# Performance work log

Hardware: AMD Instinct MI355X
Metric: run time of the kernel (lower is better)

The kernel has to match this reference:

```python
import math
import jax, jax.numpy as jnp
import numpy as np

N = 65536   # total nodes across episodes
H = 512     # hidden size
B = 4096    # number of episodes / decoding items
M = 32      # max neighbors (padded ragged valid_actions)


def setup_inputs() -> dict:
    key = jax.random.key(0)
    ks = jax.random.split(key, 9)
    s = 1.0 / math.sqrt(H)
    return {
        "h_static": jax.random.normal(ks[0], (N, H), jnp.float32),
        "h_dynamic": jax.random.normal(ks[1], (N, H), jnp.float32),
        "Ws_kvl": jax.random.normal(ks[2], (H, 3 * H), jnp.float32) * s,
        "Wd_kvl": jax.random.normal(ks[3], (H, 3 * H), jnp.float32) * s,
        "Wq": jax.random.normal(ks[4], (H, H), jnp.float32) * s,
        "batch": jax.random.randint(ks[5], (N,), 0, B, jnp.int32),
        "current_nodes": jax.random.randint(ks[6], (B,), 0, N),
        "neigh_idx": jax.random.randint(ks[7], (B, M), 0, N),
        "lengths": jax.random.randint(ks[8], (B,), 0, M + 1),
    }


def reference(h_static, h_dynamic, Ws_kvl, Wd_kvl, Wq, batch, current_nodes, neigh_idx, lengths):
    # precompute(): static KVL projection (full 3H GEMM then chunk, as in torch)
    kvl_s = h_static @ Ws_kvl            # [N, 3H]
    K_s = kvl_s[:, :H]
    # forward_batch(): dynamic projection
    kvl_d = h_dynamic @ Wd_kvl           # [N, 3H]
    K_d = kvl_d[:, :H]
    K = K_s + K_d                        # [N, H]  (V is computed but unused for outputs)
    q = (h_static[current_nodes] + h_dynamic[current_nodes]) @ Wq  # [B, H]

    # padded ragged neighbor attention (replaces the Python loop over B)
    Kn = K[neigh_idx]                                        # [B, M, H]
    compat = jnp.einsum('bmh,bh->bm', Kn, q) / math.sqrt(H)  # [B, M]
    mask = jnp.arange(M)[None, :] < lengths[:, None]         # [B, M]
    NEG = jnp.float32(-1e9)
    logits = jnp.where(mask, compat, NEG)

    # categorical sampling via Gumbel-max (Categorical(logits).sample())
    u = jax.random.uniform(jax.random.key(1), (B, M), jnp.float32, 1e-8, 1.0)
    g = -jnp.log(-jnp.log(u))
    idx = jnp.argmax(logits + g, axis=-1)                    # [B]

    logp = jax.nn.log_softmax(logits, axis=-1)               # [B, M]
    lp = jnp.take_along_axis(logp, idx[:, None], axis=1)[:, 0]
    actions = jnp.take_along_axis(neigh_idx, idx[:, None], axis=1)[:, 0]

    # empty neighbor list -> stay at current node, log_prob 0 (matches torch branch)
    nonempty = lengths > 0
    actions = jnp.where(nonempty, actions, current_nodes)
    lp = jnp.where(nonempty, lp, jnp.float32(0.0))
    return actions, lp
```

## Files before the change

kernel.cpp:

```cpp
#include <hip/hip_runtime.h>
#include <cstdint>
#include <cstddef>

#define HDIM 512
#define NM 32
#define NBATCH 4096

__device__ __forceinline__ unsigned rotl32(unsigned x, unsigned d) {
  return (x << d) | (x >> (32u - d));
}

__device__ __forceinline__ void threefry2x32(unsigned& x0, unsigned& x1) {
  const unsigned ks0 = 0u, ks1 = 1u, ks2 = 0x1BD11BDBu;
  x0 += ks0; x1 += ks1;
#define TF_RND(r) { x0 += x1; x1 = rotl32(x1, (r)); x1 ^= x0; }
  TF_RND(13) TF_RND(15) TF_RND(26) TF_RND(6)
  x0 += ks1; x1 += ks2 + 1u;
  TF_RND(17) TF_RND(29) TF_RND(16) TF_RND(24)
  x0 += ks2; x1 += ks0 + 2u;
  TF_RND(13) TF_RND(15) TF_RND(26) TF_RND(6)
  x0 += ks0; x1 += ks1 + 3u;
  TF_RND(17) TF_RND(29) TF_RND(16) TF_RND(24)
  x0 += ks1; x1 += ks2 + 4u;
  TF_RND(13) TF_RND(15) TF_RND(26) TF_RND(6)
  x0 += ks2; x1 += ks0 + 5u;
#undef TF_RND
}

__global__ void gather_hc(const float* __restrict__ hs,
                          const float* __restrict__ hd,
                          const int* __restrict__ cur,
                          float* __restrict__ Hc) {
  const int b = blockIdx.x;
  const int t = threadIdx.x;
  const int n = cur[b];
  const float4 a = ((const float4*)(hs + (size_t)n * HDIM))[t];
  const float4 c = ((const float4*)(hd + (size_t)n * HDIM))[t];
  float4 r;
  r.x = a.x + c.x; r.y = a.y + c.y; r.z = a.z + c.z; r.w = a.w + c.w;
  ((float4*)(Hc + (size_t)b * HDIM))[t] = r;
}

__global__ __launch_bounds__(256) void gemm_b1(const float* __restrict__ Ws,
                                               const float* __restrict__ Wd,
                                               const float* __restrict__ Wq,
                                               float* __restrict__ M2T) {
  constexpr int BK = 16, LDT = 68;
  __shared__ float Ast[BK][LDT];
  __shared__ float Bst[BK][LDT];
  const int tid = threadIdx.x;
  const int row0 = blockIdx.y * 64;
  const int col0 = blockIdx.x * 64;
  const float* Abase = (row0 < 512) ? Ws : Wd;
  const int arow0 = (row0 < 512) ? row0 : row0 - 512;
  const int tx = tid & 15, ty = tid >> 4;
  const int lr = tid >> 2, lc = (tid & 3) * 4;
  float acc[4][4] = {};
  for (int k0 = 0; k0 < 512; k0 += BK) {
    float4 va = *(const float4*)(Abase + (size_t)(arow0 + lr) * 1536 + k0 + lc);
    float4 vb = *(const float4*)(Wq + (size_t)(col0 + lr) * 512 + k0 + lc);
    Ast[lc + 0][lr] = va.x; Ast[lc + 1][lr] = va.y;
    Ast[lc + 2][lr] = va.z; Ast[lc + 3][lr] = va.w;
    Bst[lc + 0][lr] = vb.x; Bst[lc + 1][lr] = vb.y;
    Bst[lc + 2][lr] = vb.z; Bst[lc + 3][lr] = vb.w;
    __syncthreads();
#pragma unroll
    for (int k = 0; k < BK; ++k) {
      float4 a4 = *(const float4*)&Ast[k][ty * 4];
      float4 b4 = *(const float4*)&Bst[k][tx * 4];
      float a[4] = {a4.x, a4.y, a4.z, a4.w};
      float bb[4] = {b4.x, b4.y, b4.z, b4.w};
#pragma unroll
      for (int i = 0; i < 4; ++i)
#pragma unroll
        for (int j = 0; j < 4; ++j) acc[i][j] += a[i] * bb[j];
    }
    __syncthreads();
  }
#pragma unroll
  for (int i = 0; i < 4; ++i) {
    float4 o;
    o.x = acc[i][0]; o.y = acc[i][1]; o.z = acc[i][2]; o.w = acc[i][3];
    *(float4*)(M2T + (size_t)(row0 + ty * 4 + i) * 512 + col0 + tx * 4) = o;
  }
}

__global__ __launch_bounds__(256) void gemm_v(const float* __restrict__ A,
                                              const float* __restrict__ Bm,
                                              float* __restrict__ C) {
  constexpr int BK = 16, LDT = 132;
  __shared__ float Ast[BK][LDT];
  __shared__ float Bst[BK][LDT];
  const int tid = threadIdx.x;
  const int row0 = blockIdx.y * 128;
  const int col0 = blockIdx.x * 128;
  const int tx = tid & 15, ty = tid >> 4;
  const int lr = tid >> 2, lc = (tid & 3) * 4;
  float acc[8][8] = {};
  for (int k0 = 0; k0 < 512; k0 += BK) {
#pragma unroll
    for (int h = 0; h < 2; ++h) {
      const int r = lr + h * 64;
      float4 va = *(const float4*)(A + (size_t)(row0 + r) * 512 + k0 + lc);
      float4 vb = *(const float4*)(Bm + (size_t)(col0 + r) * 512 + k0 + lc);
      Ast[lc + 0][r] = va.x; Ast[lc + 1][r] = va.y;
      Ast[lc + 2][r] = va.z; Ast[lc + 3][r] = va.w;
      Bst[lc + 0][r] = vb.x; Bst[lc + 1][r] = vb.y;
      Bst[lc + 2][r] = vb.z; Bst[lc + 3][r] = vb.w;
    }
    __syncthreads();
#pragma unroll
    for (int k = 0; k < BK; ++k) {
      float4 a0 = *(const float4*)&Ast[k][ty * 8];
      float4 a1 = *(const float4*)&Ast[k][ty * 8 + 4];
      float4 b0 = *(const float4*)&Bst[k][tx * 8];
      float4 b1 = *(const float4*)&Bst[k][tx * 8 + 4];
      float a[8] = {a0.x, a0.y, a0.z, a0.w, a1.x, a1.y, a1.z, a1.w};
      float bb[8] = {b0.x, b0.y, b0.z, b0.w, b1.x, b1.y, b1.z, b1.w};
#pragma unroll
      for (int i = 0; i < 8; ++i)
#pragma unroll
        for (int j = 0; j < 8; ++j) acc[i][j] += a[i] * bb[j];
    }
    __syncthreads();
  }
#pragma unroll
  for (int i = 0; i < 8; ++i) {
    float4 o0, o1;
    o0.x = acc[i][0]; o0.y = acc[i][1]; o0.z = acc[i][2]; o0.w = acc[i][3];
    o1.x = acc[i][4]; o1.y = acc[i][5]; o1.z = acc[i][6]; o1.w = acc[i][7];
    float* cp = C + (size_t)(row0 + ty * 8 + i) * 1024 + col0 + tx * 8;
    *(float4*)cp = o0;
    *(float4*)(cp + 4) = o1;
  }
}

__global__ __launch_bounds__(256) void attend_kernel(
    const float* __restrict__ hs, const float* __restrict__ hd,
    const float* __restrict__ V, const int* __restrict__ neigh,
    const int* __restrict__ lengths, const int* __restrict__ cur,
    float* __restrict__ out) {
  const int b = blockIdx.x;
  const int tid = threadIdx.x;
  const int lane = tid & 63;
  const int wave = tid >> 6;
  __shared__ float compat[NM];

  const float4* vrow = (const float4*)(V + (size_t)b * (2 * HDIM));
  const float4 w0 = vrow[lane * 2], w1 = vrow[lane * 2 + 1];
  const float4 u0 = vrow[128 + lane * 2], u1 = vrow[128 + lane * 2 + 1];

#pragma unroll
  for (int mi = 0; mi < 8; ++mi) {
    const int m = wave * 8 + mi;
    const int n = neigh[b * NM + m];
    const float4* a4 = (const float4*)(hs + (size_t)n * HDIM);
    const float4* c4 = (const float4*)(hd + (size_t)n * HDIM);
    const float4 a0 = a4[lane * 2], a1 = a4[lane * 2 + 1];
    const float4 b0 = c4[lane * 2], b1 = c4[lane * 2 + 1];
    float acc = a0.x * w0.x + a0.y * w0.y + a0.z * w0.z + a0.w * w0.w
              + a1.x * w1.x + a1.y * w1.y + a1.z * w1.z + a1.w * w1.w
              + b0.x * u0.x + b0.y * u0.y + b0.z * u0.z + b0.w * u0.w
              + b1.x * u1.x + b1.y * u1.y + b1.z * u1.z + b1.w * u1.w;
#pragma unroll
    for (int off = 32; off >= 1; off >>= 1) acc += __shfl_xor(acc, off);
    if (lane == 0) compat[m] = acc;
  }
  __syncthreads();

  if (tid < 64) {
    const int len = lengths[b];
    const bool valid = tid < NM;
    const float NEGMAX = -3.402823466e38f;
    float logit = NEGMAX;
    if (valid) {
      const float cm = compat[tid] / 22.62741699796952f;
      logit = (tid < len) ? cm : -1e9f;
    }
    float z = NEGMAX;
    int zi = 1 << 20;
    if (valid) {
      const unsigned i_lo = (unsigned)b * 32u + (unsigned)tid;
      unsigned x0 = 0u;
      unsigned x1 = i_lo;
      threefry2x32(x0, x1);
      const unsigned bits = x0 ^ x1;
      const float fu = __uint_as_float((bits >> 9) | 0x3f800000u) - 1.0f;
      const float uu = fmaxf(1e-8f, fu + 1e-8f);
      const float g = -logf(-logf(uu));
      z = logit + g;
      zi = tid;
    }
#pragma unroll
    for (int off = 32; off >= 1; off >>= 1) {
      const float oz = __shfl_xor(z, off);
      const int oi = __shfl_xor(zi, off);
      if (oz > z || (oz == z && oi < zi)) { z = oz; zi = oi; }
    }
    float ml = logit;
#pragma unroll
    for (int off = 32; off >= 1; off >>= 1) ml = fmaxf(ml, __shfl_xor(ml, off));
    float ex = valid ? expf(logit - ml) : 0.f;
#pragma unroll
    for (int off = 32; off >= 1; off >>= 1) ex += __shfl_xor(ex, off);
    const float lsel = __shfl(logit, zi);
    if (tid == 0) {
      float lp = lsel - ml - logf(ex);
      int act = neigh[b * NM + zi];
      if (len <= 0) { act = cur[b]; lp = 0.f; }
      out[b] = (float)act;
      out[NBATCH + b] = lp;
    }
  }
}

extern "C" void kernel_launch(void* const* d_in, const int* in_sizes, int n_in,
                              void* d_out, int out_size, void* d_ws, size_t ws_size,
                              hipStream_t stream) {
  const float* hs = (const float*)d_in[0];
  const float* hd = (const float*)d_in[1];
  const float* Ws = (const float*)d_in[2];
  const float* Wd = (const float*)d_in[3];
  const float* Wq = (const float*)d_in[4];
  const int* cur = (const int*)d_in[6];
  const int* neigh = (const int*)d_in[7];
  const int* lens = (const int*)d_in[8];
  float* out = (float*)d_out;

  char* ws = (char*)d_ws;
  float* Hc  = (float*)ws;
  float* M2T = (float*)(ws + (size_t)NBATCH * HDIM * 4);
  float* V   = (float*)(ws + (size_t)NBATCH * HDIM * 4 + (size_t)1024 * 512 * 4);

  hipLaunchKernelGGL(gemm_b1, dim3(8, 16), dim3(256), 0, stream, Ws, Wd, Wq, M2T);
  hipLaunchKernelGGL(gather_hc, dim3(NBATCH), dim3(128), 0, stream, hs, hd, cur, Hc);
  hipLaunchKernelGGL(gemm_v, dim3(8, 32), dim3(256), 0, stream, Hc, M2T, V);
  hipLaunchKernelGGL(attend_kernel, dim3(NBATCH), dim3(256), 0, stream,
                     hs, hd, V, neigh, lens, cur, out);
}
```

Measured before the change: 185.6 us.

## Invert neighbor gather into node-centric streaming with per-node bucket index

Builds a per-node bucket of (batch, slot) entries with atomics, skipping masked slots, then streams each referenced node's h_static/h_dynamic row once and dots it against the small V rows of every batch that references it. This replaces the per-batch random gather of 32 full neighbor rows, which re-read duplicate nodes and masked entries, so far less traffic goes over the large node arrays. An overflow list handles nodes with more than CAP references, and a separate finalize kernel does the sampling and log-softmax. The cost is extra launches, a memset, atomic index building, and random reads of V rows in place of node rows.

```diff
diff --git a/kernel.cpp b/kernel.cpp
--- a/kernel.cpp
+++ b/kernel.cpp
@@ -5,6 +5,8 @@
 #define HDIM 512
 #define NM 32
 #define NBATCH 4096
+#define NNODE 65536
+#define CAP 16
 
 __device__ __forceinline__ unsigned rotl32(unsigned x, unsigned d) {
   return (x << d) | (x >> (32u - d));
@@ -135,82 +137,124 @@
   }
 }
 
-__global__ __launch_bounds__(256) void attend_kernel(
+__global__ __launch_bounds__(256) void build_index(
+    const int* __restrict__ neigh, const int* __restrict__ lens,
+    int* __restrict__ cnt, int* __restrict__ bucket,
+    int* __restrict__ ovf_cnt, int* __restrict__ ovf_list) {
+  const int t = blockIdx.x * 256 + threadIdx.x;
+  const int b = t >> 5, m = t & 31;
+  if (m < lens[b]) {
+    const int n = neigh[t];
+    const int slot = atomicAdd(&cnt[n], 1);
+    if (slot < CAP) bucket[n * CAP + slot] = t;
+    else { const int o = atomicAdd(ovf_cnt, 1); ovf_list[o] = t; }
+  }
+}
+
+__global__ __launch_bounds__(256) void stream_compat(
     const float* __restrict__ hs, const float* __restrict__ hd,
-    const float* __restrict__ V, const int* __restrict__ neigh,
-    const int* __restrict__ lengths, const int* __restrict__ cur,
-    float* __restrict__ out) {
-  const int b = blockIdx.x;
-  const int tid = threadIdx.x;
-  const int lane = tid & 63;
-  const int wave = tid >> 6;
-  __shared__ float compat[NM];
-
-  const float4* vrow = (const float4*)(V + (size_t)b * (2 * HDIM));
-  const float4 w0 = vrow[lane * 2], w1 = vrow[lane * 2 + 1];
-  const float4 u0 = vrow[128 + lane * 2], u1 = vrow[128 + lane * 2 + 1];
-
-#pragma unroll
-  for (int mi = 0; mi < 8; ++mi) {
-    const int m = wave * 8 + mi;
-    const int n = neigh[b * NM + m];
+    const float* __restrict__ V, const int* __restrict__ cnt,
+    const int* __restrict__ bucket, float* __restrict__ compat) {
+  const int n = blockIdx.x * 4 + (threadIdx.x >> 6);
+  const int lane = threadIdx.x & 63;
+  const int c = cnt[n];
+  if (c == 0) return;
+  const float4* a4 = (const float4*)(hs + (size_t)n * HDIM);
+  const float4* c4 = (const float4*)(hd + (size_t)n * HDIM);
+  const float4 a0 = a4[lane * 2], a1 = a4[lane * 2 + 1];
+  const float4 b0 = c4[lane * 2], b1 = c4[lane * 2 + 1];
+  const int cc = (c < CAP) ? c : CAP;
+  for (int e = 0; e < cc; ++e) {
+    const int t = bucket[n * CAP + e];
+    const int b = t >> 5;
+    const float4* vrow = (const float4*)(V + (size_t)b * (2 * HDIM));
+    const float4 w0 = vrow[lane * 2], w1 = vrow[lane * 2 + 1];
+    const float4 u0 = vrow[128 + lane * 2], u1 = vrow[128 + lane * 2 + 1];
+    float acc = a0.x * w0.x + a0.y * w0.y + a0.z * w0.z + a0.w * w0.w
+              + a1.x * w1.x + a1.y * w1.y + a1.z * w1.z + a1.w * w1.w
+              + b0.x * u0.x + b0.y * u0.y + b0.z * u0.z + b0.w * u0.w
+              + b1.x * u1.x + b1.y * u1.y + b1.z * u1.z + b1.w * u1.w;
+#pragma unroll
+    for (int off = 32; off >= 1; off >>= 1) acc += __shfl_xor(acc, off);
+    if (lane == 0) compat[t] = acc;
+  }
+}
+
+__global__ __launch_bounds__(256) void ovf_compat(
+    const float* __restrict__ hs, const float* __restrict__ hd,
+    const float* __restrict__ V, const int* __restrict__ ovf_cnt,
+    const int* __restrict__ ovf_list, const int* __restrict__ neigh,
+    float* __restrict__ compat) {
+  const int nw = *ovf_cnt;
+  const int lane = threadIdx.x & 63;
+  for (int e = blockIdx.x * 4 + (threadIdx.x >> 6); e < nw; e += gridDim.x * 4) {
+    const int t = ovf_list[e];
+    const int b = t >> 5;
+    const int n = neigh[t];
     const float4* a4 = (const float4*)(hs + (size_t)n * HDIM);
     const float4* c4 = (const float4*)(hd + (size_t)n * HDIM);
     const float4 a0 = a4[lane * 2], a1 = a4[lane * 2 + 1];
     const float4 b0 = c4[lane * 2], b1 = c4[lane * 2 + 1];
+    const float4* vrow = (const float4*)(V + (size_t)b * (2 * HDIM));
+    const float4 w0 = vrow[lane * 2], w1 = vrow[lane * 2 + 1];
+    const float4 u0 = vrow[128 + lane * 2], u1 = vrow[128 + lane * 2 + 1];
     float acc = a0.x * w0.x + a0.y * w0.y + a0.z * w0.z + a0.w * w0.w
               + a1.x * w1.x + a1.y * w1.y + a1.z * w1.z + a1.w * w1.w
               + b0.x * u0.x + b0.y * u0.y + b0.z * u0.z + b0.w * u0.w
               + b1.x * u1.x + b1.y * u1.y + b1.z * u1.z + b1.w * u1.w;
 #pragma unroll
     for (int off = 32; off >= 1; off >>= 1) acc += __shfl_xor(acc, off);
-    if (lane == 0) compat[m] = acc;
-  }
-  __syncthreads();
-
-  if (tid < 64) {
-    const int len = lengths[b];
-    const bool valid = tid < NM;
-    const float NEGMAX = -3.402823466e38f;
-    float logit = NEGMAX;
-    if (valid) {
-      const float cm = compat[tid] / 22.62741699796952f;
-      logit = (tid < len) ? cm : -1e9f;
-    }
-    float z = NEGMAX;
-    int zi = 1 << 20;
-    if (valid) {
-      const unsigned i_lo = (unsigned)b * 32u + (unsigned)tid;
-      unsigned x0 = 0u;
-      unsigned x1 = i_lo;
-      threefry2x32(x0, x1);
-      const unsigned bits = x0 ^ x1;
-      const float fu = __uint_as_float((bits >> 9) | 0x3f800000u) - 1.0f;
-      const float uu = fmaxf(1e-8f, fu + 1e-8f);
-      const float g = -logf(-logf(uu));
-      z = logit + g;
-      zi = tid;
-    }
-#pragma unroll
-    for (int off = 32; off >= 1; off >>= 1) {
-      const float oz = __shfl_xor(z, off);
-      const int oi = __shfl_xor(zi, off);
-      if (oz > z || (oz == z && oi < zi)) { z = oz; zi = oi; }
-    }
-    float ml = logit;
-#pragma unroll
-    for (int off = 32; off >= 1; off >>= 1) ml = fmaxf(ml, __shfl_xor(ml, off));
-    float ex = valid ? expf(logit - ml) : 0.f;
-#pragma unroll
-    for (int off = 32; off >= 1; off >>= 1) ex += __shfl_xor(ex, off);
-    const float lsel = __shfl(logit, zi);
-    if (tid == 0) {
-      float lp = lsel - ml - logf(ex);
-      int act = neigh[b * NM + zi];
-      if (len <= 0) { act = cur[b]; lp = 0.f; }
-      out[b] = (float)act;
-      out[NBATCH + b] = lp;
-    }
+    if (lane == 0) compat[t] = acc;
+  }
+}
+
+__global__ __launch_bounds__(256) void finalize_kernel(
+    const float* __restrict__ compat, const int* __restrict__ neigh,
+    const int* __restrict__ lengths, const int* __restrict__ cur,
+    float* __restrict__ out) {
+  const int b = blockIdx.x * 4 + (threadIdx.x >> 6);
+  const int tid = threadIdx.x & 63;
+  const int len = lengths[b];
+  const bool valid = tid < NM;
+  const float NEGMAX = -3.402823466e38f;
+  float logit = NEGMAX;
+  if (valid) {
+    const float cm = compat[b * NM + tid] / 22.62741699796952f;
+    logit = (tid < len) ? cm : -1e9f;
+  }
+  float z = NEGMAX;
+  int zi = 1 << 20;
+  if (valid) {
+    const unsigned i_lo = (unsigned)b * 32u + (unsigned)tid;
+    unsigned x0 = 0u;
+    unsigned x1 = i_lo;
+    threefry2x32(x0, x1);
+    const unsigned bits = x0 ^ x1;
+    const float fu = __uint_as_float((bits >> 9) | 0x3f800000u) - 1.0f;
+    const float uu = fmaxf(1e-8f, fu + 1e-8f);
+    const float g = -logf(-logf(uu));
+    z = logit + g;
+    zi = tid;
+  }
+#pragma unroll
+  for (int off = 32; off >= 1; off >>= 1) {
+    const float oz = __shfl_xor(z, off);
+    const int oi = __shfl_xor(zi, off);
+    if (oz > z || (oz == z && oi < zi)) { z = oz; zi = oi; }
+  }
+  float ml = logit;
+#pragma unroll
+  for (int off = 32; off >= 1; off >>= 1) ml = fmaxf(ml, __shfl_xor(ml, off));
+  float ex = valid ? expf(logit - ml) : 0.f;
+#pragma unroll
+  for (int off = 32; off >= 1; off >>= 1) ex += __shfl_xor(ex, off);
+  const float lsel = __shfl(logit, zi);
+  if (tid == 0) {
+    float lp = lsel - ml - logf(ex);
+    int act = neigh[b * NM + zi];
+    if (len <= 0) { act = cur[b]; lp = 0.f; }
+    out[b] = (float)act;
+    out[NBATCH + b] = lp;
   }
 }
 
@@ -228,13 +272,26 @@
   float* out = (float*)d_out;
 
   char* ws = (char*)d_ws;
-  float* Hc  = (float*)ws;
-  float* M2T = (float*)(ws + (size_t)NBATCH * HDIM * 4);
-  float* V   = (float*)(ws + (size_t)NBATCH * HDIM * 4 + (size_t)1024 * 512 * 4);
-
+  size_t off = 0;
+  int* cnt = (int*)(ws + off);        off += (size_t)NNODE * 4;
+  int* ovf_cnt = (int*)(ws + off);    off += 256;
+  int* bucket = (int*)(ws + off);     off += (size_t)NNODE * CAP * 4;
+  int* ovf_list = (int*)(ws + off);   off += (size_t)NBATCH * NM * 4;
+  float* compat = (float*)(ws + off); off += (size_t)NBATCH * NM * 4;
+  float* Hc = (float*)(ws + off);     off += (size_t)NBATCH * HDIM * 4;
+  float* M2T = (float*)(ws + off);    off += (size_t)1024 * 512 * 4;
+  float* V = (float*)(ws + off);      off += (size_t)NBATCH * 2 * HDIM * 4;
+
+  hipMemsetAsync(cnt, 0, (size_t)NNODE * 4 + 256, stream);
+  hipLaunchKernelGGL(build_index, dim3(NBATCH * NM / 256), dim3(256), 0, stream,
+                     neigh, lens, cnt, bucket, ovf_cnt, ovf_list);
   hipLaunchKernelGGL(gemm_b1, dim3(8, 16), dim3(256), 0, stream, Ws, Wd, Wq, M2T);
   hipLaunchKernelGGL(gather_hc, dim3(NBATCH), dim3(128), 0, stream, hs, hd, cur, Hc);
   hipLaunchKernelGGL(gemm_v, dim3(8, 32), dim3(256), 0, stream, Hc, M2T, V);
-  hipLaunchKernelGGL(attend_kernel, dim3(NBATCH), dim3(256), 0, stream,
-                     hs, hd, V, neigh, lens, cur, out);
-}
+  hipLaunchKernelGGL(stream_compat, dim3(NNODE / 4), dim3(256), 0, stream,
+                     hs, hd, V, cnt, bucket, compat);
+  hipLaunchKernelGGL(ovf_compat, dim3(32), dim3(256), 0, stream,
+                     hs, hd, V, ovf_cnt, ovf_list, neigh, compat);
+  hipLaunchKernelGGL(finalize_kernel, dim3(NBATCH / 4), dim3(256), 0, stream,
+                     compat, neigh, lens, cur, out);
+}
```

Result: faster. 177.9 us (-4.1%).
